# Performance work log

Measured on AMD Instinct MI355X. Metric: run time of the kernel, lower is better.

## Reference

```python
import jax, jax.numpy as jnp
import numpy as np

EPS = 1e-8


def setup_inputs() -> dict:
    key = jax.random.key(0)
    k1, k2, k3, k4 = jax.random.split(key, 4)
    B, N, M, C = 512, 512, 128, 1024
    addr = M + 6  # read head: k(M) + beta(1) + g(1) + s(3) + gamma(1)
    controller_out = jax.random.normal(k1, (B, C), dtype=jnp.float32)
    prev_w = jax.random.uniform(k2, (B, N), dtype=jnp.float32)
    prev_w = prev_w / prev_w.sum(axis=1, keepdims=True)  # valid weighting
    memory_state = jax.random.normal(k3, (B, N, M), dtype=jnp.float32)
    W_fc = jax.random.normal(k4, (C, addr), dtype=jnp.float32) * 0.02
    b_fc = jnp.zeros((addr,), dtype=jnp.float32)
    return {"controller_out": controller_out, "prev_w": prev_w,
            "memory_state": memory_state, "W_fc": W_fc, "b_fc": b_fc}


def reference(controller_out, prev_w, memory_state, W_fc, b_fc):
    M = memory_state.shape[2]
    out = controller_out @ W_fc + b_fc  # [B, M+6]
    k = out[:, :M]                                   # key
    beta = jax.nn.softplus(out[:, M:M + 1])          # key strength
    g = jax.nn.sigmoid(out[:, M + 1:M + 2])          # interpolation gate
    s = jax.nn.softmax(out[:, M + 2:M + 5], axis=1)  # 3-tap shift weights
    gamma = 1.0 + jax.nn.softplus(out[:, M + 5:M + 6])

    # Content addressing (Eq. 5-6): cosine similarity + sharpened softmax
    norm_k = jnp.linalg.norm(k, axis=1, keepdims=True) + EPS      # [B,1]
    norm_mem = jnp.linalg.norm(memory_state, axis=2) + EPS        # [B,N]
    sim = jnp.einsum('bnm,bm->bn', memory_state, k) / (norm_k * norm_mem)
    w_c = jax.nn.softmax(beta * sim, axis=1)

    # Interpolation (Eq. 7)
    w_g = g * w_c + (1.0 - g) * prev_w

    # Circular 3-tap shift (Eq. 8): vectorized roll instead of per-slot loop
    w_s = (s[:, 0:1] * jnp.roll(w_g, 1, axis=1)
           + s[:, 1:2] * w_g
           + s[:, 2:3] * jnp.roll(w_g, -1, axis=1))

    # Sharpening (Eq. 9)
    w_pow = w_s ** gamma
    w = w_pow / (w_pow.sum(axis=1, keepdims=True) + EPS)

    # Read vector (read head)
    read_vec = jnp.einsum('bn,bnm->bm', w, memory_state)
    return (read_vec, w)
```

## Files before the change

kernel.cpp:

```cpp
#include <hip/hip_runtime.h>
#include <math.h>
#include <float.h>

#define BB   512
#define NN   512
#define MM   128
#define CC   1024
#define ADDR 134
#define EPSF 1e-8f

__device__ __forceinline__ float softplus_f(float x) {
    return fmaxf(x, 0.0f) + log1pf(expf(-fabsf(x)));
}

__global__ __launch_bounds__(1024, 8) void ntm_head_kernel(
    const float* __restrict__ co,
    const float* __restrict__ prev_w,
    const float* __restrict__ mem,
    const float* __restrict__ W_fc,
    const float* __restrict__ b_fc,
    float* __restrict__ out_rv,
    float* __restrict__ out_w)
{
    __shared__ __align__(16) float s_co[CC];
    __shared__ __align__(16) float s_k[MM];
    __shared__ float s_extra[8];
    __shared__ __align__(16) float s_bsim[NN];
    __shared__ float s_wg[NN];
    __shared__ float s_w[NN];
    __shared__ __align__(16) float s_part[32 * MM];
    __shared__ float s_red[16];
    __shared__ float s_params[8];

    const int t = threadIdx.x;
    const int b = blockIdx.x;

    s_co[t] = co[(size_t)b * CC + t];

    float pw = 0.0f;
    if (t < NN) pw = prev_w[(size_t)b * NN + t];

    __syncthreads();

    {
        const int o    = t & (MM - 1);
        const int part = t >> 7;
        const float* Wp = W_fc + o;
        float a0 = 0.f, a1 = 0.f, a2 = 0.f, a3 = 0.f;
        const int c0 = part * (CC / 8);
        for (int c = c0; c < c0 + CC / 8; c += 4) {
            float4 cv = *(const float4*)(s_co + c);
            a0 = fmaf(cv.x, Wp[(size_t)(c + 0) * ADDR], a0);
            a1 = fmaf(cv.y, Wp[(size_t)(c + 1) * ADDR], a1);
            a2 = fmaf(cv.z, Wp[(size_t)(c + 2) * ADDR], a2);
            a3 = fmaf(cv.w, Wp[(size_t)(c + 3) * ADDR], a3);
        }
        s_part[part * MM + o] = (a0 + a1) + (a2 + a3);

        const int wv = t >> 6;
        if (wv < 6) {
            const int l  = t & 63;
            const int oe = MM + wv;
            const float* We = W_fc + oe;
            float e = 0.f;
            for (int c = l; c < CC; c += 64)
                e = fmaf(s_co[c], We[(size_t)c * ADDR], e);
            #pragma unroll
            for (int off = 32; off >= 1; off >>= 1) e += __shfl_xor(e, off, 64);
            if (l == 0) s_extra[wv] = e + b_fc[oe];
        }
    }
    __syncthreads();

    if (t < MM) {
        float r = b_fc[t];
        #pragma unroll
        for (int p = 0; p < 8; ++p) r += s_part[p * MM + t];
        s_k[t] = r;
        float v = r * r;
        #pragma unroll
        for (int off = 32; off >= 1; off >>= 1) v += __shfl_xor(v, off, 64);
        if ((t & 63) == 0) s_red[t >> 6] = v;
    }
    __syncthreads();
    if (t == 0) {
        float ks = s_red[0] + s_red[1];
        float norm_k = sqrtf(ks) + EPSF;
        float beta = softplus_f(s_extra[0]);
        float g = 1.0f / (1.0f + expf(-s_extra[1]));
        float e0 = s_extra[2], e1 = s_extra[3], e2 = s_extra[4];
        float mx = fmaxf(e0, fmaxf(e1, e2));
        float x0 = expf(e0 - mx), x1 = expf(e1 - mx), x2 = expf(e2 - mx);
        float inv = 1.0f / (x0 + x1 + x2);
        s_params[0] = beta / norm_k;
        s_params[1] = g;
        s_params[2] = x0 * inv;
        s_params[3] = x1 * inv;
        s_params[4] = x2 * inv;
        s_params[5] = 1.0f + softplus_f(s_extra[5]);
    }
    __syncthreads();

    const float bnk = s_params[0];
    const float4* memb = (const float4*)(mem + (size_t)b * NN * MM);
    const int gi = t >> 5;
    const int l  = t & 31;

    {
        float4 kv = ((const float4*)s_k)[l];
        for (int j = 0; j < 16; j += 4) {
            const int r0 = gi + (j    ) * 32;
            const int r1 = gi + (j + 1) * 32;
            const int r2 = gi + (j + 2) * 32;
            const int r3 = gi + (j + 3) * 32;
            float4 a0 = memb[r0 * 32 + l];
            float4 a1 = memb[r1 * 32 + l];
            float4 a2 = memb[r2 * 32 + l];
            float4 a3 = memb[r3 * 32 + l];
            float d0 = a0.x*kv.x + a0.y*kv.y + a0.z*kv.z + a0.w*kv.w;
            float q0 = a0.x*a0.x + a0.y*a0.y + a0.z*a0.z + a0.w*a0.w;
            float d1 = a1.x*kv.x + a1.y*kv.y + a1.z*kv.z + a1.w*kv.w;
            float q1 = a1.x*a1.x + a1.y*a1.y + a1.z*a1.z + a1.w*a1.w;
            float d2 = a2.x*kv.x + a2.y*kv.y + a2.z*kv.z + a2.w*kv.w;
            float q2 = a2.x*a2.x + a2.y*a2.y + a2.z*a2.z + a2.w*a2.w;
            float d3 = a3.x*kv.x + a3.y*kv.y + a3.z*kv.z + a3.w*kv.w;
            float q3 = a3.x*a3.x + a3.y*a3.y + a3.z*a3.z + a3.w*a3.w;
            #pragma unroll
            for (int off = 16; off >= 1; off >>= 1) {
                d0 += __shfl_xor(d0, off, 64); q0 += __shfl_xor(q0, off, 64);
                d1 += __shfl_xor(d1, off, 64); q1 += __shfl_xor(q1, off, 64);
                d2 += __shfl_xor(d2, off, 64); q2 += __shfl_xor(q2, off, 64);
                d3 += __shfl_xor(d3, off, 64); q3 += __shfl_xor(q3, off, 64);
            }
            if (l == 0) {
                s_bsim[r0] = bnk * d0 / (sqrtf(q0) + EPSF);
                s_bsim[r1] = bnk * d1 / (sqrtf(q1) + EPSF);
                s_bsim[r2] = bnk * d2 / (sqrtf(q2) + EPSF);
                s_bsim[r3] = bnk * d3 / (sqrtf(q3) + EPSF);
            }
        }
    }
    __syncthreads();

    {
        const float NEG = -3.0e38f;
        float b1 = (t < NN) ? s_bsim[t] : NEG;

        float m = b1;
        #pragma unroll
        for (int off = 32; off >= 1; off >>= 1) m = fmaxf(m, __shfl_xor(m, off, 64));
        if ((t & 63) == 0) s_red[t >> 6] = m;
        __syncthreads();
        float M8 = s_red[0];
        #pragma unroll
        for (int i = 1; i < 8; ++i) M8 = fmaxf(M8, s_red[i]);
        __syncthreads();

        float e1 = (t < NN) ? expf(b1 - M8) : 0.0f;
        float ls = e1;
        #pragma unroll
        for (int off = 32; off >= 1; off >>= 1) ls += __shfl_xor(ls, off, 64);
        if ((t & 63) == 0) s_red[t >> 6] = ls;
        __syncthreads();
        float S = s_red[0];
        #pragma unroll
        for (int i = 1; i < 8; ++i) S += s_red[i];
        __syncthreads();

        const float invS = 1.0f / S;
        const float g = s_params[1];
        float wg1 = fmaf(g, e1 * invS, (1.0f - g) * pw);
        if (t < NN) s_wg[t] = wg1;
        __syncthreads();

        const float sh0 = s_params[2], sh1 = s_params[3], sh2 = s_params[4];
        const float gamma = s_params[5];
        float wp1 = 0.0f;
        if (t < NN) {
            float ws1 = sh0 * s_wg[(t + NN - 1) & (NN - 1)]
                      + sh1 * wg1
                      + sh2 * s_wg[(t + 1) & (NN - 1)];
            wp1 = powf(ws1, gamma);
        }
        float lz = wp1;
        #pragma unroll
        for (int off = 32; off >= 1; off >>= 1) lz += __shfl_xor(lz, off, 64);
        if ((t & 63) == 0) s_red[t >> 6] = lz;
        __syncthreads();
        float Z = s_red[0];
        #pragma unroll
        for (int i = 1; i < 8; ++i) Z += s_red[i];
        __syncthreads();

        const float invZ = 1.0f / (Z + EPSF);
        if (t < NN) {
            float w1 = wp1 * invZ;
            s_w[t] = w1;
            out_w[(size_t)b * NN + t] = w1;
        }
    }
    __syncthreads();

    {
        float4 acc = make_float4(0.f, 0.f, 0.f, 0.f);
        for (int j = 0; j < 16; j += 4) {
            const int r0 = gi + (j    ) * 32;
            const int r1 = gi + (j + 1) * 32;
            const int r2 = gi + (j + 2) * 32;
            const int r3 = gi + (j + 3) * 32;
            float4 a0 = memb[r0 * 32 + l];
            float4 a1 = memb[r1 * 32 + l];
            float4 a2 = memb[r2 * 32 + l];
            float4 a3 = memb[r3 * 32 + l];
            float w0 = s_w[r0], w1 = s_w[r1], w2 = s_w[r2], w3 = s_w[r3];
            acc.x = fmaf(w0, a0.x, acc.x); acc.y = fmaf(w0, a0.y, acc.y);
            acc.z = fmaf(w0, a0.z, acc.z); acc.w = fmaf(w0, a0.w, acc.w);
            acc.x = fmaf(w1, a1.x, acc.x); acc.y = fmaf(w1, a1.y, acc.y);
            acc.z = fmaf(w1, a1.z, acc.z); acc.w = fmaf(w1, a1.w, acc.w);
            acc.x = fmaf(w2, a2.x, acc.x); acc.y = fmaf(w2, a2.y, acc.y);
            acc.z = fmaf(w2, a2.z, acc.z); acc.w = fmaf(w2, a2.w, acc.w);
            acc.x = fmaf(w3, a3.x, acc.x); acc.y = fmaf(w3, a3.y, acc.y);
            acc.z = fmaf(w3, a3.z, acc.z); acc.w = fmaf(w3, a3.w, acc.w);
        }
        *((float4*)&s_part[gi * MM + l * 4]) = acc;
        __syncthreads();

        if (t < 512) {
            const int h = t >> 7;
            const int o = t & (MM - 1);
            float r = 0.f;
            #pragma unroll
            for (int q = 0; q < 8; ++q) r += s_part[(h * 8 + q) * MM + o];
            s_bsim[h * MM + o] = r;
        }
        __syncthreads();
        if (t < MM) {
            float r = s_bsim[t] + s_bsim[MM + t] + s_bsim[2 * MM + t] + s_bsim[3 * MM + t];
            out_rv[(size_t)b * MM + t] = r;
        }
    }
}

extern "C" void kernel_launch(void* const* d_in, const int* in_sizes, int n_in,
                              void* d_out, int out_size, void* d_ws, size_t ws_size,
                              hipStream_t stream) {
    const float* co     = (const float*)d_in[0];
    const float* prev_w = (const float*)d_in[1];
    const float* mem    = (const float*)d_in[2];
    const float* W_fc   = (const float*)d_in[3];
    const float* b_fc   = (const float*)d_in[4];
    float* out = (float*)d_out;
    ntm_head_kernel<<<BB, 1024, 0, stream>>>(co, prev_w, mem, W_fc, b_fc,
                                             out, out + (size_t)BB * MM);
}
```

Baseline: 227.6 us.

## Software-pipeline memory row loads and prefetch across phase barriers

Memory rows are now register-prefetched: the first batch of the similarity pass is issued before the parameter-reduction barriers so it overlaps the FC matvec tail, and later batches are double-buffered in the unrolled loop. The first batch for the read-vector pass is likewise issued before the softmax/shift/sharpen phases. The per-row result write is spread across lanes 0-3 instead of one lane doing four divides. This hides global-load latency behind compute and syncs, at the cost of more registers in a 1024-thread block.

```diff
diff --git a/kernel.cpp b/kernel.cpp
--- a/kernel.cpp
+++ b/kernel.cpp
@@ -1,6 +1,5 @@
 #include <hip/hip_runtime.h>
 #include <math.h>
-#include <float.h>
 
 #define BB   512
 #define NN   512
@@ -34,12 +33,12 @@
 
     const int t = threadIdx.x;
     const int b = blockIdx.x;
+    const int gi = t >> 5;
+    const int l  = t & 31;
+    const float4* memb = (const float4*)(mem + (size_t)b * NN * MM);
 
     s_co[t] = co[(size_t)b * CC + t];
-
-    float pw = 0.0f;
-    if (t < NN) pw = prev_w[(size_t)b * NN + t];
-
+    float pw = (t < NN) ? prev_w[(size_t)b * NN + t] : 0.0f;
     __syncthreads();
 
     {
@@ -59,17 +58,23 @@
 
         const int wv = t >> 6;
         if (wv < 6) {
-            const int l  = t & 63;
+            const int ll = t & 63;
             const int oe = MM + wv;
             const float* We = W_fc + oe;
             float e = 0.f;
-            for (int c = l; c < CC; c += 64)
+            for (int c = ll; c < CC; c += 64)
                 e = fmaf(s_co[c], We[(size_t)c * ADDR], e);
             #pragma unroll
             for (int off = 32; off >= 1; off >>= 1) e += __shfl_xor(e, off, 64);
-            if (l == 0) s_extra[wv] = e + b_fc[oe];
-        }
-    }
+            if (ll == 0) s_extra[wv] = e + b_fc[oe];
+        }
+    }
+
+    float4 p0 = memb[(size_t)(gi      ) * 32 + l];
+    float4 p1 = memb[(size_t)(gi + 32 ) * 32 + l];
+    float4 p2 = memb[(size_t)(gi + 64 ) * 32 + l];
+    float4 p3 = memb[(size_t)(gi + 96 ) * 32 + l];
+
     __syncthreads();
 
     if (t < MM) {
@@ -102,44 +107,44 @@
     __syncthreads();
 
     const float bnk = s_params[0];
-    const float4* memb = (const float4*)(mem + (size_t)b * NN * MM);
-    const int gi = t >> 5;
-    const int l  = t & 31;
-
-    {
-        float4 kv = ((const float4*)s_k)[l];
-        for (int j = 0; j < 16; j += 4) {
-            const int r0 = gi + (j    ) * 32;
-            const int r1 = gi + (j + 1) * 32;
-            const int r2 = gi + (j + 2) * 32;
-            const int r3 = gi + (j + 3) * 32;
-            float4 a0 = memb[r0 * 32 + l];
-            float4 a1 = memb[r1 * 32 + l];
-            float4 a2 = memb[r2 * 32 + l];
-            float4 a3 = memb[r3 * 32 + l];
-            float d0 = a0.x*kv.x + a0.y*kv.y + a0.z*kv.z + a0.w*kv.w;
-            float q0 = a0.x*a0.x + a0.y*a0.y + a0.z*a0.z + a0.w*a0.w;
-            float d1 = a1.x*kv.x + a1.y*kv.y + a1.z*kv.z + a1.w*kv.w;
-            float q1 = a1.x*a1.x + a1.y*a1.y + a1.z*a1.z + a1.w*a1.w;
-            float d2 = a2.x*kv.x + a2.y*kv.y + a2.z*kv.z + a2.w*kv.w;
-            float q2 = a2.x*a2.x + a2.y*a2.y + a2.z*a2.z + a2.w*a2.w;
-            float d3 = a3.x*kv.x + a3.y*kv.y + a3.z*kv.z + a3.w*kv.w;
-            float q3 = a3.x*a3.x + a3.y*a3.y + a3.z*a3.z + a3.w*a3.w;
-            #pragma unroll
-            for (int off = 16; off >= 1; off >>= 1) {
-                d0 += __shfl_xor(d0, off, 64); q0 += __shfl_xor(q0, off, 64);
-                d1 += __shfl_xor(d1, off, 64); q1 += __shfl_xor(q1, off, 64);
-                d2 += __shfl_xor(d2, off, 64); q2 += __shfl_xor(q2, off, 64);
-                d3 += __shfl_xor(d3, off, 64); q3 += __shfl_xor(q3, off, 64);
-            }
-            if (l == 0) {
-                s_bsim[r0] = bnk * d0 / (sqrtf(q0) + EPSF);
-                s_bsim[r1] = bnk * d1 / (sqrtf(q1) + EPSF);
-                s_bsim[r2] = bnk * d2 / (sqrtf(q2) + EPSF);
-                s_bsim[r3] = bnk * d3 / (sqrtf(q3) + EPSF);
-            }
-        }
-    }
+    const float4 kv = ((const float4*)s_k)[l];
+
+    #pragma unroll
+    for (int j = 0; j < 16; j += 4) {
+        float4 a0 = p0, a1 = p1, a2 = p2, a3 = p3;
+        if (j + 4 < 16) {
+            p0 = memb[(size_t)(gi + (j + 4) * 32) * 32 + l];
+            p1 = memb[(size_t)(gi + (j + 5) * 32) * 32 + l];
+            p2 = memb[(size_t)(gi + (j + 6) * 32) * 32 + l];
+            p3 = memb[(size_t)(gi + (j + 7) * 32) * 32 + l];
+        }
+        float d0 = a0.x*kv.x + a0.y*kv.y + a0.z*kv.z + a0.w*kv.w;
+        float q0 = a0.x*a0.x + a0.y*a0.y + a0.z*a0.z + a0.w*a0.w;
+        float d1 = a1.x*kv.x + a1.y*kv.y + a1.z*kv.z + a1.w*kv.w;
+        float q1 = a1.x*a1.x + a1.y*a1.y + a1.z*a1.z + a1.w*a1.w;
+        float d2 = a2.x*kv.x + a2.y*kv.y + a2.z*kv.z + a2.w*kv.w;
+        float q2 = a2.x*a2.x + a2.y*a2.y + a2.z*a2.z + a2.w*a2.w;
+        float d3 = a3.x*kv.x + a3.y*kv.y + a3.z*kv.z + a3.w*kv.w;
+        float q3 = a3.x*a3.x + a3.y*a3.y + a3.z*a3.z + a3.w*a3.w;
+        #pragma unroll
+        for (int off = 16; off >= 1; off >>= 1) {
+            d0 += __shfl_xor(d0, off, 64); q0 += __shfl_xor(q0, off, 64);
+            d1 += __shfl_xor(d1, off, 64); q1 += __shfl_xor(q1, off, 64);
+            d2 += __shfl_xor(d2, off, 64); q2 += __shfl_xor(q2, off, 64);
+            d3 += __shfl_xor(d3, off, 64); q3 += __shfl_xor(q3, off, 64);
+        }
+        float dd = d0, qq = q0; int rr = gi + j * 32;
+        if (l == 1) { dd = d1; qq = q1; rr = gi + (j + 1) * 32; }
+        if (l == 2) { dd = d2; qq = q2; rr = gi + (j + 2) * 32; }
+        if (l == 3) { dd = d3; qq = q3; rr = gi + (j + 3) * 32; }
+        if (l < 4) s_bsim[rr] = bnk * dd / (sqrtf(qq) + EPSF);
+    }
+
+    p0 = memb[(size_t)(gi      ) * 32 + l];
+    p1 = memb[(size_t)(gi + 32 ) * 32 + l];
+    p2 = memb[(size_t)(gi + 64 ) * 32 + l];
+    p3 = memb[(size_t)(gi + 96 ) * 32 + l];
+
     __syncthreads();
 
     {
@@ -203,15 +208,19 @@
 
     {
         float4 acc = make_float4(0.f, 0.f, 0.f, 0.f);
+        #pragma unroll
         for (int j = 0; j < 16; j += 4) {
+            float4 a0 = p0, a1 = p1, a2 = p2, a3 = p3;
             const int r0 = gi + (j    ) * 32;
             const int r1 = gi + (j + 1) * 32;
             const int r2 = gi + (j + 2) * 32;
             const int r3 = gi + (j + 3) * 32;
-            float4 a0 = memb[r0 * 32 + l];
-            float4 a1 = memb[r1 * 32 + l];
-            float4 a2 = memb[r2 * 32 + l];
-            float4 a3 = memb[r3 * 32 + l];
+            if (j + 4 < 16) {
+                p0 = memb[(size_t)(gi + (j + 4) * 32) * 32 + l];
+                p1 = memb[(size_t)(gi + (j + 5) * 32) * 32 + l];
+                p2 = memb[(size_t)(gi + (j + 6) * 32) * 32 + l];
+                p3 = memb[(size_t)(gi + (j + 7) * 32) * 32 + l];
+            }
             float w0 = s_w[r0], w1 = s_w[r1], w2 = s_w[r2], w3 = s_w[r3];
             acc.x = fmaf(w0, a0.x, acc.x); acc.y = fmaf(w0, a0.y, acc.y);
             acc.z = fmaf(w0, a0.z, acc.z); acc.w = fmaf(w0, a0.w, acc.w);
```

Measured after the change: 228.8 us. Within noise of the previous version (+0.6%).
